# Performance work log

Measured on AMD Instinct MI355X. Metric: run time of the kernel, lower is better.

The kernel has to match this reference:

```python
import jax, jax.numpy as jnp
import numpy as np

E = 8          # expert_num
H = 1024       # hidden_size
I = 4096       # intermediate_size
T = 4096       # token_num (sum of per-expert loads)
CAP = 1024     # static per-expert capacity bound (>= max load)


def setup_inputs() -> dict:
    key = jax.random.key(0)
    k1, k2, k3, k4, k5 = jax.random.split(key, 5)
    inter_state = jax.random.normal(k1, (T, H), dtype=jnp.float32)
    # variable per-expert capacities, sum == T, each <= CAP
    loads = jnp.array([600, 450, 550, 500, 512, 520, 450, 514], dtype=jnp.int32)
    # nn.Linear weights stored pre-transposed for right-multiplication: y = x @ W + b
    W1 = jax.random.normal(k2, (E, H, I), dtype=jnp.float32) * (1.0 / np.sqrt(H))
    b1 = jax.random.normal(k3, (E, I), dtype=jnp.float32) * 0.02
    W2 = jax.random.normal(k4, (E, I, H), dtype=jnp.float32) * (1.0 / np.sqrt(I))
    b2 = jax.random.normal(k5, (E, H), dtype=jnp.float32) * 0.02
    return {"inter_state": inter_state, "loads": loads,
            "W1": W1, "b1": b1, "W2": W2, "b2": b2}


def _grouped_ffn(x, loads, W1, b1, W2, b2):
    # Tokens are laid out contiguously per expert (grouped GEMM with variable
    # capacities). Dispatch into a padded [E, CAP, H] buffer (static shapes,
    # jit-safe), run the two per-expert GEMMs + exact GELU, gather back.
    tok = jnp.arange(T)
    ends = jnp.cumsum(loads)                      # [E] segment ends
    eid = jnp.searchsorted(ends, tok, side="right")  # [T] expert id per token
    pos = tok - (ends[eid] - loads[eid])             # position within segment
    buf = jnp.zeros((E, CAP, H), x.dtype).at[eid, pos].set(x)  # [E,CAP,H]
    h = jnp.einsum("ech,ehi->eci", buf, W1) + b1[:, None, :]   # expert GEMM 1
    h = jax.nn.gelu(h, approximate=False)                      # unfused act pass
    out = jnp.einsum("eci,eih->ech", h, W2) + b2[:, None, :]   # expert GEMM 2
    return out[eid, pos]                                       # [T, H]


def reference(inter_state, loads, W1, b1, W2, b2):
    return _grouped_ffn(inter_state, loads, W1, b1, W2, b2)
```

## Files before the change

### kernel.cpp

```cpp
#include <hip/hip_runtime.h>
#include <hip/hip_bf16.h>

#define E_ 8
#define H_ 1024
#define I_ 4096
#define T_ 4096
#define CAP_ 1024

typedef __attribute__((ext_vector_type(8))) short bf16x8;
typedef __attribute__((ext_vector_type(4))) float f32x4;

__device__ __forceinline__ unsigned short f2bf(float f) {
  union { float f; unsigned int u; } v; v.f = f;
  unsigned int r = v.u + 0x7FFFu + ((v.u >> 16) & 1u);
  return (unsigned short)(r >> 16);
}

__device__ __forceinline__ void gload16(const void* g, void* l) {
  __builtin_amdgcn_global_load_lds(
      (const __attribute__((address_space(1))) unsigned int*)g,
      (__attribute__((address_space(3))) unsigned int*)l, 16, 0, 0);
}

__device__ __forceinline__ void cvt_body(const float* __restrict__ in,
                                         unsigned short* __restrict__ out,
                                         int n4, int bid, int nblocks) {
  int i = bid * 256 + threadIdx.x;
  const int stride = nblocks * 256;
  for (; i < n4; i += stride) {
    float4 v = ((const float4*)in)[i];
    ushort4 o;
    o.x = f2bf(v.x); o.y = f2bf(v.y); o.z = f2bf(v.z); o.w = f2bf(v.w);
    ((ushort4*)out)[i] = o;
  }
}

__global__ void init_out(float* __restrict__ out, const float* __restrict__ b2,
                         const int* __restrict__ loads) {
  const int idx = blockIdx.x * blockDim.x + threadIdx.x;
  if (idx >= T_ * H_ / 4) return;
  const int row = idx >> 8;
  const int c4 = (idx & 255) * 4;
  int acc = 0, e = 0;
#pragma unroll
  for (int i = 0; i < E_; ++i) {
    int li = loads[i];
    if (row >= acc + li) e = i + 1;
    acc += li;
  }
  float4 b = *(const float4*)&b2[(size_t)e * H_ + c4];
  ((float4*)out)[idx] = b;
}

__global__ void reduce_out(const float* __restrict__ partials,
                           const float* __restrict__ b2,
                           const int* __restrict__ loads,
                           float* __restrict__ out) {
  const int idx = blockIdx.x * blockDim.x + threadIdx.x;
  if (idx >= T_ * H_ / 4) return;
  const int row = idx >> 8;
  const int c4 = (idx & 255) * 4;
  int acc = 0, e = 0;
#pragma unroll
  for (int i = 0; i < E_; ++i) {
    int li = loads[i];
    if (row >= acc + li) e = i + 1;
    acc += li;
  }
  float4 s = *(const float4*)&b2[(size_t)e * H_ + c4];
  constexpr size_t STRIDE4 = (size_t)T_ * H_ / 4;
#pragma unroll
  for (int ks = 0; ks < 4; ++ks) {
    float4 p = ((const float4*)partials)[ks * STRIDE4 + idx];
    s.x += p.x; s.y += p.y; s.z += p.z; s.w += p.w;
  }
  ((float4*)out)[idx] = s;
}

__device__ __forceinline__ void transpose_tile(const float* __restrict__ A,
                                               unsigned short* __restrict__ B,
                                               int R, int C, int r0, int c0) {
  __shared__ float tile[64][65];
  const int t = threadIdx.x;
#pragma unroll
  for (int p = 0; p < 4; ++p) {
    int r = (t >> 4) + p * 16;
    int c = (t & 15) * 4;
    float4 v = *(const float4*)&A[(size_t)(r0 + r) * C + (c0 + c)];
    tile[r][c + 0] = v.x; tile[r][c + 1] = v.y;
    tile[r][c + 2] = v.z; tile[r][c + 3] = v.w;
  }
  __syncthreads();
#pragma unroll
  for (int p = 0; p < 4; ++p) {
    int c  = (t >> 4) + p * 16;
    int rr = (t & 15) * 4;
    ushort4 o;
    o.x = f2bf(tile[rr + 0][c]);
    o.y = f2bf(tile[rr + 1][c]);
    o.z = f2bf(tile[rr + 2][c]);
    o.w = f2bf(tile[rr + 3][c]);
    *(ushort4*)&B[(size_t)(c0 + c) * R + (r0 + rr)] = o;
  }
}

__global__ __launch_bounds__(256) void fused_cvt_t1(
    const float* __restrict__ x, unsigned short* __restrict__ x_bf,
    const float* __restrict__ W1, unsigned short* __restrict__ w1t) {
  const int bid = blockIdx.x;
  if (bid < 512) {
    cvt_body(x, x_bf, (T_ * H_) / 4, bid, 512);
  } else {
    const int tt = bid - 512;
    const int e = tt >> 10, rem = tt & 1023;
    transpose_tile(W1 + (size_t)e * H_ * I_, w1t + (size_t)e * H_ * I_,
                   H_, I_, (rem & 15) * 64, (rem >> 4) * 64);
  }
}

template <int K, int N, int KSPLIT, int EPI>
__device__ __forceinline__ void gemm_tile(
    const unsigned short* __restrict__ Abase,
    const unsigned short* __restrict__ BT,
    const float* __restrict__ bias,
    const int* __restrict__ loads,
    void* __restrict__ out_ptr,
    int e, int mtile, int ntile, int ks) {
  __shared__ unsigned short lds_a[128 * 32];
  __shared__ unsigned short lds_b[128 * 32];
  constexpr int KCH = K / KSPLIT;

  int seg0 = 0, load_e = 0;
#pragma unroll
  for (int i = 0; i < E_; ++i) {
    int li = loads[i];
    seg0 += (i < e) ? li : 0;
    if (i == e) load_e = li;
  }
  const int row0 = mtile * 128;
  if (row0 >= load_e) return;
  const int ncol0 = ntile * 128;

  const int t = threadIdx.x;
  const int lane = t & 63;
  const int w = t >> 6;
  const int wr = w >> 1, wc = w & 1;

  const unsigned short* Bexp = BT + (size_t)e * N * K;

  f32x4 acc[4][4];
#pragma unroll
  for (int i = 0; i < 4; ++i)
#pragma unroll
    for (int j = 0; j < 4; ++j) acc[i][j] = (f32x4){0.f, 0.f, 0.f, 0.f};

  const unsigned short* gA[2];
  const unsigned short* gB[2];
  unsigned short* ldsA[2];
  unsigned short* ldsB[2];
#pragma unroll
  for (int it = 0; it < 2; ++it) {
    int c = it * 256 + t;
    int rowi = c >> 2, off = (c & 3) * 8;
    int gr = seg0 + row0 + rowi;
    if (gr > T_ - 1) gr = T_ - 1;
    gA[it] = Abase + (size_t)gr * K + ks * KCH + off;
    gB[it] = Bexp + (size_t)(ncol0 + rowi) * K + ks * KCH + off;
    ldsA[it] = &lds_a[(size_t)(it * 256 + w * 64) * 8];
    ldsB[it] = &lds_b[(size_t)(it * 256 + w * 64) * 8];
  }

  const int r = lane & 15, kq = lane >> 4;

  for (int kt = 0; kt < KCH / 32; ++kt) {
    const int kb = kt * 32;
#pragma unroll
    for (int it = 0; it < 2; ++it) {
      gload16(gA[it] + kb, ldsA[it]);
      gload16(gB[it] + kb, ldsB[it]);
    }
    __syncthreads();
    bf16x8 av[4], bv[4];
#pragma unroll
    for (int mi = 0; mi < 4; ++mi)
      av[mi] = *(const bf16x8*)&lds_a[(wr * 64 + mi * 16 + r) * 32 + kq * 8];
#pragma unroll
    for (int ni = 0; ni < 4; ++ni)
      bv[ni] = *(const bf16x8*)&lds_b[(wc * 64 + ni * 16 + r) * 32 + kq * 8];
#pragma unroll
    for (int mi = 0; mi < 4; ++mi)
#pragma unroll
      for (int ni = 0; ni < 4; ++ni)
        acc[mi][ni] = __builtin_amdgcn_mfma_f32_16x16x32_bf16(
            av[mi], bv[ni], acc[mi][ni], 0, 0, 0);
    __syncthreads();
  }

  const int r4 = (lane >> 4) * 4;
  const int cc = lane & 15;
  const bool full_tile = (row0 + 128 <= load_e);
  float* outf = (float*)out_ptr;
  if constexpr (EPI == 1) outf += (size_t)ks * T_ * N;
#pragma unroll
  for (int ni = 0; ni < 4; ++ni) {
    const int col = ncol0 + wc * 64 + ni * 16 + cc;
    float bv = 0.f;
    if constexpr (EPI == 0) bv = bias[(size_t)e * N + col];
#pragma unroll
    for (int mi = 0; mi < 4; ++mi) {
#pragma unroll
      for (int rr = 0; rr < 4; ++rr) {
        const int rowl = row0 + wr * 64 + mi * 16 + r4 + rr;
        if (full_tile || rowl < load_e) {
          float v = acc[mi][ni][rr] + bv;
          const size_t o = (size_t)(seg0 + rowl) * N + col;
          if constexpr (EPI == 0) {
            v = 0.5f * v * (1.0f + erff(v * 0.70710678118f));
            ((unsigned short*)out_ptr)[o] = f2bf(v);
          } else if constexpr (EPI == 1) {
            outf[o] = v;
          } else {
            unsafeAtomicAdd(&outf[o], v);
          }
        }
      }
    }
  }
}

template <int K, int N, int KSPLIT, int EPI>
__global__ __launch_bounds__(256) void grouped_gemm(
    const unsigned short* __restrict__ Abase,
    const unsigned short* __restrict__ BT,
    const float* __restrict__ bias,
    const int* __restrict__ loads,
    void* __restrict__ out_ptr) {
  gemm_tile<K, N, KSPLIT, EPI>(Abase, BT, bias, loads, out_ptr,
                               (int)blockIdx.z / KSPLIT, (int)blockIdx.y,
                               (int)blockIdx.x, (int)blockIdx.z % KSPLIT);
}

__global__ __launch_bounds__(256) void fused_g1_t2(
    const unsigned short* __restrict__ x_bf,
    const unsigned short* __restrict__ w1t,
    const float* __restrict__ b1,
    const int* __restrict__ loads,
    unsigned short* __restrict__ hbuf,
    const float* __restrict__ W2,
    unsigned short* __restrict__ w2t) {
  const int bid = blockIdx.x;
  const int sel = bid % 5;
  if (sel == 4) {
    const int g = bid / 5;
    const int e = g >> 8, rem = g & 255;
    gemm_tile<H_, I_, 1, 0>(x_bf, w1t, b1, loads, (void*)hbuf,
                            e, rem >> 5, rem & 31, 0);
  } else {
    const int tt = (bid / 5) * 4 + sel;
    const int e = tt >> 10, rem = tt & 1023;
    transpose_tile(W2 + (size_t)e * I_ * H_, w2t + (size_t)e * I_ * H_,
                   I_, H_, (rem >> 4) * 64, (rem & 15) * 64);
  }
}

extern "C" void kernel_launch(void* const* d_in, const int* in_sizes, int n_in,
                              void* d_out, int out_size, void* d_ws,
                              size_t ws_size, hipStream_t stream) {
  const float* x = (const float*)d_in[0];
  const int* loads = (const int*)d_in[1];
  const float* W1 = (const float*)d_in[2];
  const float* b1 = (const float*)d_in[3];
  const float* W2 = (const float*)d_in[4];
  const float* b2 = (const float*)d_in[5];
  float* out = (float*)d_out;

  char* ws = (char*)d_ws;
  unsigned short* x_bf = (unsigned short*)(ws);
  unsigned short* w1t  = (unsigned short*)(ws + ((size_t)8 << 20));
  unsigned short* w2t  = (unsigned short*)(ws + ((size_t)72 << 20));
  unsigned short* hbuf = (unsigned short*)(ws + ((size_t)136 << 20));
  float* partials      = (float*)(ws + ((size_t)168 << 20));
  const bool use_partials = ws_size >= ((size_t)232 << 20);

  if (!use_partials)
    init_out<<<(T_ * H_ / 4 + 255) / 256, 256, 0, stream>>>(out, b2, loads);
  fused_cvt_t1<<<8704, 256, 0, stream>>>(x, x_bf, W1, w1t);
  fused_g1_t2<<<10240, 256, 0, stream>>>(x_bf, w1t, b1, loads, hbuf, W2, w2t);
  if (use_partials) {
    grouped_gemm<I_, H_, 4, 1>
        <<<dim3(H_ / 128, CAP_ / 128, E_ * 4), 256, 0, stream>>>(
            hbuf, w2t, nullptr, loads, (void*)partials);
    reduce_out<<<(T_ * H_ / 4 + 255) / 256, 256, 0, stream>>>(partials, b2,
                                                              loads, out);
  } else {
    grouped_gemm<I_, H_, 4, 2>
        <<<dim3(H_ / 128, CAP_ / 128, E_ * 4), 256, 0, stream>>>(
            hbuf, w2t, nullptr, loads, out);
  }
}
```

Baseline: 482.0 us.

## Share one LDS buffer between fused branches and raise MFMA wave priority

```diff
diff --git a/kernel.cpp b/kernel.cpp
--- a/kernel.cpp
+++ b/kernel.cpp
@@ -6,6 +6,8 @@
 #define I_ 4096
 #define T_ 4096
 #define CAP_ 1024
+
+#define SMEM_BYTES 16640
 
 typedef __attribute__((ext_vector_type(8))) short bf16x8;
 typedef __attribute__((ext_vector_type(4))) float f32x4;
@@ -79,8 +81,9 @@
 
 __device__ __forceinline__ void transpose_tile(const float* __restrict__ A,
                                                unsigned short* __restrict__ B,
-                                               int R, int C, int r0, int c0) {
-  __shared__ float tile[64][65];
+                                               int R, int C, int r0, int c0,
+                                               char* smem) {
+  float (*tile)[65] = (float(*)[65])smem;
   const int t = threadIdx.x;
 #pragma unroll
   for (int p = 0; p < 4; ++p) {
@@ -107,6 +110,7 @@
 __global__ __launch_bounds__(256) void fused_cvt_t1(
     const float* __restrict__ x, unsigned short* __restrict__ x_bf,
     const float* __restrict__ W1, unsigned short* __restrict__ w1t) {
+  __shared__ __align__(16) char smem[SMEM_BYTES];
   const int bid = blockIdx.x;
   if (bid < 512) {
     cvt_body(x, x_bf, (T_ * H_) / 4, bid, 512);
@@ -114,20 +118,20 @@
     const int tt = bid - 512;
     const int e = tt >> 10, rem = tt & 1023;
     transpose_tile(W1 + (size_t)e * H_ * I_, w1t + (size_t)e * H_ * I_,
-                   H_, I_, (rem & 15) * 64, (rem >> 4) * 64);
-  }
-}
-
-template <int K, int N, int KSPLIT, int EPI>
+                   H_, I_, (rem & 15) * 64, (rem >> 4) * 64, smem);
+  }
+}
+
+template <int K, int N, int KSPLIT, int EPI, bool SETPRIO>
 __device__ __forceinline__ void gemm_tile(
     const unsigned short* __restrict__ Abase,
     const unsigned short* __restrict__ BT,
     const float* __restrict__ bias,
     const int* __restrict__ loads,
     void* __restrict__ out_ptr,
-    int e, int mtile, int ntile, int ks) {
-  __shared__ unsigned short lds_a[128 * 32];
-  __shared__ unsigned short lds_b[128 * 32];
+    int e, int mtile, int ntile, int ks, char* smem) {
+  unsigned short* lds_a = (unsigned short*)smem;
+  unsigned short* lds_b = (unsigned short*)(smem + 8192);
   constexpr int KCH = K / KSPLIT;
 
   int seg0 = 0, load_e = 0;
@@ -187,12 +191,14 @@
 #pragma unroll
     for (int ni = 0; ni < 4; ++ni)
       bv[ni] = *(const bf16x8*)&lds_b[(wc * 64 + ni * 16 + r) * 32 + kq * 8];
+    if constexpr (SETPRIO) __builtin_amdgcn_s_setprio(1);
 #pragma unroll
     for (int mi = 0; mi < 4; ++mi)
 #pragma unroll
       for (int ni = 0; ni < 4; ++ni)
         acc[mi][ni] = __builtin_amdgcn_mfma_f32_16x16x32_bf16(
             av[mi], bv[ni], acc[mi][ni], 0, 0, 0);
+    if constexpr (SETPRIO) __builtin_amdgcn_s_setprio(0);
     __syncthreads();
   }
 
@@ -235,9 +241,10 @@
     const float* __restrict__ bias,
     const int* __restrict__ loads,
     void* __restrict__ out_ptr) {
-  gemm_tile<K, N, KSPLIT, EPI>(Abase, BT, bias, loads, out_ptr,
-                               (int)blockIdx.z / KSPLIT, (int)blockIdx.y,
-                               (int)blockIdx.x, (int)blockIdx.z % KSPLIT);
+  __shared__ __align__(16) char smem[16384];
+  gemm_tile<K, N, KSPLIT, EPI, false>(
+      Abase, BT, bias, loads, out_ptr, (int)blockIdx.z / KSPLIT,
+      (int)blockIdx.y, (int)blockIdx.x, (int)blockIdx.z % KSPLIT, smem);
 }
 
 __global__ __launch_bounds__(256) void fused_g1_t2(
@@ -248,18 +255,19 @@
     unsigned short* __restrict__ hbuf,
     const float* __restrict__ W2,
     unsigned short* __restrict__ w2t) {
+  __shared__ __align__(16) char smem[SMEM_BYTES];
   const int bid = blockIdx.x;
   const int sel = bid % 5;
   if (sel == 4) {
     const int g = bid / 5;
     const int e = g >> 8, rem = g & 255;
-    gemm_tile<H_, I_, 1, 0>(x_bf, w1t, b1, loads, (void*)hbuf,
-                            e, rem >> 5, rem & 31, 0);
+    gemm_tile<H_, I_, 1, 0, true>(x_bf, w1t, b1, loads, (void*)hbuf,
+                                  e, rem >> 5, rem & 31, 0, smem);
   } else {
     const int tt = (bid / 5) * 4 + sel;
     const int e = tt >> 10, rem = tt & 1023;
     transpose_tile(W2 + (size_t)e * I_ * H_, w2t + (size_t)e * I_ * H_,
-                   I_, H_, (rem >> 4) * 64, (rem & 15) * 64);
+                   I_, H_, (rem >> 4) * 64, (rem & 15) * 64, smem);
   }
 }
 
```

After: 480.7 us. No clear change (-0.3%).
